# Performance work log

Hardware: AMD Instinct MI355X
Metric: run time of the kernel (lower is better)

## Reference

```python
import jax, jax.numpy as jnp
from jax import lax
import numpy as np

B = 16; C1 = 96; H4 = 28; W4 = 64
FULL_H = 448; FULL_W = 1024
BACKWARP = 1.25   # fltBackwarp for intLevel=4
SCALE = 16.0      # 2**intLevel
MD = 4            # correlation max displacement -> (2*MD+1)**2 = 81 channels


def _lrelu(x):
    return jnp.where(x >= 0, x, 0.1 * x)


def _conv3(x, w, b):
    y = lax.conv_general_dilated(x, w, (1, 1), [(1, 1), (1, 1)],
                                 dimension_numbers=('NCHW', 'OIHW', 'NCHW'))
    return y + b[None, :, None, None]


def _deconv4s2(x, w, b):
    # PyTorch ConvTranspose2d(k=4, s=2, p=1); w has PyTorch layout (in, out, kH, kW)
    wt = jnp.transpose(w[:, :, ::-1, ::-1], (1, 0, 2, 3))  # flipped, (out, in, kH, kW)
    y = lax.conv_general_dilated(x, wt, (1, 1), [(2, 2), (2, 2)],
                                 lhs_dilation=(2, 2),
                                 dimension_numbers=('NCHW', 'OIHW', 'NCHW'))
    return y + b[None, :, None, None]


def _correlation(f1, f2):
    # Channel-mean cost volume over a (2*MD+1)^2 displacement window.
    b, c, h, w = f1.shape
    f2p = jnp.pad(f2, ((0, 0), (0, 0), (MD, MD), (MD, MD)))
    vols = [jnp.mean(f1 * f2p[:, :, dy:dy + h, dx:dx + w], axis=1)
            for dy in range(2 * MD + 1) for dx in range(2 * MD + 1)]
    return jnp.stack(vols, axis=1)  # [B, 81, H, W]


def _warp(feat, flow):
    # Bilinear backward warp with zero padding outside the image.
    b, c, h, w = feat.shape
    gy, gx = jnp.meshgrid(jnp.arange(h, dtype=feat.dtype),
                          jnp.arange(w, dtype=feat.dtype), indexing='ij')
    x = gx[None] + flow[:, 0]
    y = gy[None] + flow[:, 1]
    x0 = jnp.floor(x); y0 = jnp.floor(y)
    wx = x - x0; wy = y - y0
    feat_flat = feat.reshape(b, c, h * w)

    def gather(yi, xi):
        valid = ((yi >= 0) & (yi <= h - 1) & (xi >= 0) & (xi <= w - 1)).astype(feat.dtype)
        yc = jnp.clip(yi, 0, h - 1).astype(jnp.int32)
        xc = jnp.clip(xi, 0, w - 1).astype(jnp.int32)
        idx = (yc * w + xc).reshape(b, 1, h * w)
        g = jnp.take_along_axis(feat_flat, jnp.broadcast_to(idx, (b, c, h * w)), axis=2)
        return g.reshape(b, c, h, w) * valid[:, None]

    return (gather(y0, x0) * ((1 - wy) * (1 - wx))[:, None]
            + gather(y0, x0 + 1) * ((1 - wy) * wx)[:, None]
            + gather(y0 + 1, x0) * (wy * (1 - wx))[:, None]
            + gather(y0 + 1, x0 + 1) * (wy * wx)[:, None])


def _quat_to_mat(q):
    # (w, x, y, z) quaternion -> rotation matrix, pytorch3d convention.
    q = q / jnp.linalg.norm(q, axis=-1, keepdims=True)
    w, x, y, z = q[:, 0], q[:, 1], q[:, 2], q[:, 3]
    R = jnp.stack([
        1 - 2 * (y * y + z * z), 2 * (x * y - w * z),     2 * (x * z + w * y),
        2 * (x * y + w * z),     1 - 2 * (x * x + z * z), 2 * (y * z - w * x),
        2 * (x * z - w * y),     2 * (y * z + w * x),     1 - 2 * (x * x + y * y)
    ], axis=-1).reshape(-1, 3, 3)
    return R


def _rot_flow(R, K, Kinv, h, w):
    # Rotational flow: p' = K R K^{-1} p (homogeneous), flow = p'/z - p.
    gy, gx = jnp.meshgrid(jnp.arange(h, dtype=R.dtype),
                          jnp.arange(w, dtype=R.dtype), indexing='ij')
    p = jnp.stack([gx.ravel(), gy.ravel(), jnp.ones(h * w, dtype=R.dtype)], axis=0)  # [3, HW]
    M = jnp.einsum('ij,bjk,kl->bil', K, R, Kinv)  # [B,3,3]
    pp = jnp.einsum('bij,jn->bin', M, p)
    pp2 = pp[:, :2] / pp[:, 2:3]
    return (pp2 - p[None, :2]).reshape(-1, 2, h, w)


def setup_inputs():
    key = jax.random.key(0)
    ks = jax.random.split(key, 24)

    def rnd(i, shape, scale=1.0):
        return scale * jax.random.normal(ks[i], shape, dtype=jnp.float32)

    def wconv(i, cout, cin, k=3):
        return rnd(i, (cout, cin, k, k), (2.0 / (cin * k * k)) ** 0.5)

    K = np.array([[500.0, 0.0, FULL_W / 2.0],
                  [0.0, 500.0, FULL_H / 2.0],
                  [0.0, 0.0, 1.0]], dtype=np.float32)
    quat = jnp.concatenate([jnp.ones((B, 1), jnp.float32), 0.01 * rnd(0, (B, 3))], axis=1)
    return {
        'tenOne': rnd(1, (B, C1, H4, W4)),
        'tenTwo': rnd(2, (B, C1, H4, W4)),
        'prev_flow': rnd(3, (B, 2, H4 // 2, W4 // 2)),
        'prev_feat': rnd(4, (B, 663, H4 // 2, W4 // 2)),
        'rotation_quat': quat,
        'cam_intri': jnp.asarray(K),
        'cam_intri_inv': jnp.asarray(np.linalg.inv(K)),
        'upflow_w': rnd(5, (2, 2, 4, 4), 0.1),
        'upflow_b': jnp.zeros((2,), jnp.float32),
        'upfeat_w': rnd(6, (663, 2, 4, 4), 0.02),
        'upfeat_b': jnp.zeros((2,), jnp.float32),
        'w1': wconv(7, 128, 183), 'b1': jnp.zeros((128,), jnp.float32),
        'w2': wconv(8, 128, 311), 'b2': jnp.zeros((128,), jnp.float32),
        'w3': wconv(9, 96, 439),  'b3': jnp.zeros((96,), jnp.float32),
        'w4': wconv(10, 64, 535), 'b4': jnp.zeros((64,), jnp.float32),
        'w5': wconv(11, 32, 599), 'b5': jnp.zeros((32,), jnp.float32),
        'w6': wconv(12, 2, 631),  'b6': jnp.zeros((2,), jnp.float32),
        'height': FULL_H,
        'width': FULL_W,
    }


def reference(tenOne, tenTwo, prev_flow, prev_feat, rotation_quat, cam_intri, cam_intri_inv,
              upflow_w, upflow_b, upfeat_w, upfeat_b,
              w1, b1, w2, b2, w3, b3, w4, b4, w5, b5, w6, b6, height, width):
    rh, rw = height // 16, width // 16  # 2**intLevel = 16
    delt_R = _quat_to_mat(rotation_quat)
    R_flow = _rot_flow(delt_R, cam_intri, cam_intri_inv, height, width)
    R_flow_r = jax.image.resize(R_flow, (R_flow.shape[0], 2, rh, rw), method='bilinear') / SCALE
    tenTwo_w = _warp(tenTwo, R_flow_r)
    tenFlow = _deconv4s2(prev_flow, upflow_w, upflow_b)
    tenFeatUp = _deconv4s2(prev_feat, upfeat_w, upfeat_b)
    tenVolume = _lrelu(_correlation(tenOne, _warp(tenTwo_w, tenFlow * BACKWARP)))
    feat = jnp.concatenate([tenVolume, R_flow_r, tenOne, tenFlow, tenFeatUp], axis=1)  # 183 ch
    for wc, bc in ((w1, b1), (w2, b2), (w3, b3), (w4, b4), (w5, b5)):
        feat = jnp.concatenate([_lrelu(_conv3(feat, wc, bc)), feat], axis=1)
    tenFlow_out = _lrelu(_conv3(feat, w6, b6))
    return tenFlow_out, feat
```

## Files before the change

kernel.cpp:

```cpp
#include <hip/hip_runtime.h>
#include <cstdint>
#include <cstddef>

typedef unsigned short u16;
typedef __attribute__((ext_vector_type(8))) short  short8;
typedef __attribute__((ext_vector_type(4))) float  f32x4;

#define HW4   1792
#define FCH   631
#define OUTOFF ((size_t)57344)

__device__ __forceinline__ float b2f(u16 u){
  union { unsigned int i; float f; } v; v.i = ((unsigned int)u) << 16; return v.f;
}
__device__ __forceinline__ u16 f2b(float f){
  unsigned int x = __float_as_uint(f);
  return (u16)((x + 0x7fffu + ((x >> 16) & 1u)) >> 16);
}
__device__ __forceinline__ float lrelu(float v){ return v >= 0.f ? v : 0.1f * v; }
__device__ __forceinline__ bool is_f32(const void* probe){ return ((const float*)probe)[0] > 1.0f; }
__device__ __forceinline__ float ldg_(const void* p, size_t i, bool f){
  return f ? ((const float*)p)[i] : b2f(((const u16*)p)[i]);
}
__device__ __forceinline__ void stg_(void* p, size_t i, float v, bool f){
  if (f) ((float*)p)[i] = v; else ((u16*)p)[i] = f2b(v);
}
__device__ __forceinline__ short8 zero8(){
  union { long long l[2]; short8 s; } z; z.l[0] = 0; z.l[1] = 0; return z.s;
}
__device__ __forceinline__ f32x4 zero4(){
  union { long long l[2]; f32x4 s; } z; z.l[0] = 0; z.l[1] = 0; return z.s;
}
__device__ __forceinline__ short8 swap16(short8 v){
  union { short8 s; unsigned int u[4]; } a, r;
  a.s = v;
  #pragma unroll
  for (int i = 0; i < 4; i++) r.u[i] = (a.u[i] >> 16) | (a.u[i] << 16);
  return r.s;
}

__global__ void k_M(const void* __restrict__ quat, const void* __restrict__ K,
                    const void* __restrict__ Kinv, float* __restrict__ Mout){
  bool f = is_f32(K);
  int b = threadIdx.x;
  if (b >= 16) return;
  float q0 = ldg_(quat,b*4+0,f), q1 = ldg_(quat,b*4+1,f);
  float q2 = ldg_(quat,b*4+2,f), q3 = ldg_(quat,b*4+3,f);
  float n = sqrtf(q0*q0 + q1*q1 + q2*q2 + q3*q3);
  float w = q0/n, x = q1/n, y = q2/n, z = q3/n;
  float R[9];
  R[0] = 1.f - 2.f*(y*y + z*z); R[1] = 2.f*(x*y - w*z); R[2] = 2.f*(x*z + w*y);
  R[3] = 2.f*(x*y + w*z); R[4] = 1.f - 2.f*(x*x + z*z); R[5] = 2.f*(y*z - w*x);
  R[6] = 2.f*(x*z - w*y); R[7] = 2.f*(y*z + w*x); R[8] = 1.f - 2.f*(x*x + y*y);
  float Kf[9], Ki[9];
  for (int i = 0; i < 9; i++){ Kf[i] = ldg_(K,i,f); Ki[i] = ldg_(Kinv,i,f); }
  float T[9];
  for (int r = 0; r < 3; r++)
    for (int c = 0; c < 3; c++)
      T[r*3+c] = R[r*3+0]*Ki[0*3+c] + R[r*3+1]*Ki[1*3+c] + R[r*3+2]*Ki[2*3+c];
  for (int r = 0; r < 3; r++)
    for (int c = 0; c < 3; c++)
      Mout[b*9 + r*3 + c] = Kf[r*3+0]*T[0*3+c] + Kf[r*3+1]*T[1*3+c] + Kf[r*3+2]*T[2*3+c];
}

__global__ void k_rflow_col(const float* __restrict__ Mws, float* __restrict__ tmpA){
  int t = blockIdx.x * 256 + threadIdx.x;
  int xo = t & 63;
  int yf = (t >> 6) % 448;
  int b  = t / (448*64);
  const float* M = Mws + b*9;
  float m0=M[0],m1=M[1],m2=M[2],m3=M[3],m4=M[4],m5=M[5],m6=M[6],m7=M[7],m8=M[8];
  float cx = 16.f*xo + 7.5f;
  float yff = (float)yf;
  float su = 0.f, sv = 0.f, wsum = 0.f;
  for (int i = 0; i < 32; i++){
    int xi = 16*xo - 8 + i;
    if (xi < 0 || xi > 1023) continue;
    float xf = (float)xi;
    float wgt = 1.f - fabsf(xf - cx) * (1.f/16.f);
    float den = m6*xf + m7*yff + m8;
    float inv = 1.f / den;
    float u = (m0*xf + m1*yff + m2)*inv - xf;
    float v = (m3*xf + m4*yff + m5)*inv - yff;
    su += wgt*u; sv += wgt*v; wsum += wgt;
  }
  float rn = 1.f / wsum;
  tmpA[((size_t)(b*2+0)*64 + xo)*448 + yf] = su*rn;
  tmpA[((size_t)(b*2+1)*64 + xo)*448 + yf] = sv*rn;
}

__global__ void k_rflow_row(const float* __restrict__ tmpA, float* __restrict__ rfr,
                            void* __restrict__ outb, const void* probe){
  bool f = is_f32(probe);
  int t = blockIdx.x * 256 + threadIdx.x;
  int xo = t & 63;
  int yo = (t >> 6) % 28;
  int b  = t / HW4;
  float cy = 16.f*yo + 7.5f;
  for (int c = 0; c < 2; c++){
    const float* col = tmpA + ((size_t)(b*2+c)*64 + xo)*448;
    float s = 0.f, wsum = 0.f;
    for (int i = 0; i < 32; i++){
      int yi = 16*yo - 8 + i;
      if (yi < 0 || yi > 447) continue;
      float wgt = 1.f - fabsf((float)yi - cy) * (1.f/16.f);
      s += wgt * col[yi]; wsum += wgt;
    }
    float val = s / (wsum * 16.0f);
    rfr[(size_t)(b*2+c)*HW4 + yo*64 + xo] = val;
    stg_(outb, OUTOFF + ((size_t)b*FCH + 529 + c)*HW4 + yo*64 + xo, val, f);
  }
}

__global__ void k_dflow(const void* __restrict__ pf, const void* __restrict__ w,
                        const void* __restrict__ bias, float* __restrict__ tflow,
                        void* __restrict__ outb, const void* probe){
  bool f = is_f32(probe);
  int t = blockIdx.x * 256 + threadIdx.x;
  int x = t & 63;
  int y = (t >> 6) % 28;
  int co = (t / HW4) & 1;
  int b  = t / (2*HW4);
  float acc = ldg_(bias, co, f);
  for (int ky = 0; ky < 4; ky++){
    int dy = y + ky - 2;
    if (dy < 0 || dy > 26 || (dy & 1)) continue;
    int iy = dy >> 1;
    for (int kx = 0; kx < 4; kx++){
      int dx = x + kx - 2;
      if (dx < 0 || dx > 62 || (dx & 1)) continue;
      int ix = dx >> 1;
      for (int ci = 0; ci < 2; ci++){
        acc += ldg_(pf, ((size_t)(b*2+ci)*14 + iy)*32 + ix, f) *
               ldg_(w,  (size_t)ci*32 + co*16 + (3-ky)*4 + (3-kx), f);
      }
    }
  }
  tflow[(size_t)(b*2+co)*HW4 + y*64 + x] = acc;
  stg_(outb, OUTOFF + ((size_t)b*FCH + 627 + co)*HW4 + y*64 + x, acc, f);
}

#define DF_NCH 42
__global__ __launch_bounds__(256) void k_dfeat_s1(
    const void* __restrict__ pfeat, const void* __restrict__ w,
    float* __restrict__ part, const void* probe){
  bool f = is_f32(probe);
  __shared__ float s_in[16*448];
  __shared__ float s_w[16*32];
  const int tid = threadIdx.x;
  const int ch = blockIdx.x;
  const int b  = blockIdx.y;
  if (f){
    const float* src = (const float*)pfeat + ((size_t)b*663 + (size_t)ch*16)*448;
    #pragma unroll
    for (int i = 0; i < 7; i++){
      int e = tid + 256*i;
      int ci = ch*16 + e/112;
      float4 v = {0.f,0.f,0.f,0.f};
      if (ci < 663) v = *(const float4*)(src + e*4);
      *(float4*)&s_in[e*4] = v;
    }
  } else {
    const u16* src = (const u16*)pfeat + ((size_t)b*663 + (size_t)ch*16)*448;
    #pragma unroll
    for (int i = 0; i < 7; i++){
      int e = tid + 256*i;
      int ci = ch*16 + e/112;
      float4 v = {0.f,0.f,0.f,0.f};
      if (ci < 663){
        ushort4 u = *(const ushort4*)(src + e*4);
        v.x = b2f(u.x); v.y = b2f(u.y); v.z = b2f(u.z); v.w = b2f(u.w);
      }
      *(float4*)&s_in[e*4] = v;
    }
  }
  #pragma unroll
  for (int i = 0; i < 2; i++){
    int e = tid + 256*i;
    int ci = ch*16 + (e >> 5);
    s_w[e] = (ci < 663) ? ldg_(w, (size_t)ci*32 + (e & 31), f) : 0.f;
  }
  __syncthreads();
  const int x = tid & 63;
  int ix0=-1, ix1=-1, wx0=0, wx1=0;
  { int n = 0;
    for (int kx = (x & 1); kx < 4; kx += 2){
      int dx = x + kx - 2;
      if (dx >= 0 && dx <= 62){
        if (n == 0){ ix0 = dx >> 1; wx0 = 3-kx; } else { ix1 = dx >> 1; wx1 = 3-kx; }
        n++;
      }
    } }
  float* pout = part + (size_t)(b*DF_NCH + ch)*2*1792;
  #pragma unroll
  for (int i = 0; i < 7; i++){
    int p = tid + 256*i;
    int y = p >> 6;
    int iy0=-1, iy1=-1, wy0=0, wy1=0;
    { int n = 0;
      for (int ky = (y & 1); ky < 4; ky += 2){
        int dy = y + ky - 2;
        if (dy >= 0 && dy <= 26){
          if (n == 0){ iy0 = dy >> 1; wy0 = (3-ky)*4; } else { iy1 = dy >> 1; wy1 = (3-ky)*4; }
          n++;
        }
      } }
    const bool v00 = (iy0 >= 0) && (ix0 >= 0);
    const bool v01 = (iy0 >= 0) && (ix1 >= 0);
    const bool v10 = (iy1 >= 0) && (ix0 >= 0);
    const bool v11 = (iy1 >= 0) && (ix1 >= 0);
    const int o00 = iy0*32+ix0, o01 = iy0*32+ix1, o10 = iy1*32+ix0, o11 = iy1*32+ix1;
    const int w00 = wy0+wx0, w01 = wy0+wx1, w10 = wy1+wx0, w11 = wy1+wx1;
    float a0 = 0.f, a1 = 0.f;
    #pragma unroll 4
    for (int ci = 0; ci < 16; ci++){
      const float* si = s_in + ci*448;
      const float* sw = s_w + ci*32;
      if (v00){ float iv = si[o00]; a0 += iv*sw[w00]; a1 += iv*sw[16+w00]; }
      if (v01){ float iv = si[o01]; a0 += iv*sw[w01]; a1 += iv*sw[16+w01]; }
      if (v10){ float iv = si[o10]; a0 += iv*sw[w10]; a1 += iv*sw[16+w10]; }
      if (v11){ float iv = si[o11]; a0 += iv*sw[w11]; a1 += iv*sw[16+w11]; }
    }
    pout[p]        = a0;
    pout[1792 + p] = a1;
  }
}

__global__ void k_dfeat_s2(const float* __restrict__ part, const void* __restrict__ bias,
                           void* __restrict__ outb, const void* probe){
  bool f = is_f32(probe);
  int t = blockIdx.x * 256 + threadIdx.x;
  int x = t & 63;
  int y = (t >> 6) % 28;
  int co = (t / HW4) & 1;
  int b  = t / (2*HW4);
  float s = ldg_(bias, co, f);
  const float* pp = part + ((size_t)b*(2*DF_NCH) + co)*1792 + (size_t)(y*64 + x);
  #pragma unroll
  for (int ch = 0; ch < DF_NCH; ch++) s += pp[(size_t)ch*3584];
  stg_(outb, OUTOFF + ((size_t)b*FCH + 629 + co)*HW4 + y*64 + x, s, f);
}

__global__ void k_copy_one(const void* __restrict__ one, void* __restrict__ outb,
                           const void* probe){
  bool f = is_f32(probe);
  int t = blockIdx.x * 256 + threadIdx.x;
  int p = t % HW4;
  int c = (t / HW4) % 96;
  int b = t / (96*HW4);
  stg_(outb, OUTOFF + ((size_t)b*FCH + 531 + c)*HW4 + p,
       ldg_(one, (size_t)(b*96+c)*HW4 + p, f), f);
}

__global__ void k_warp2(const void* __restrict__ two, const float* __restrict__ rfr,
                        const float* __restrict__ tflow, float* __restrict__ wrp2,
                        const void* probe){
  bool f = is_f32(probe);
  int t = blockIdx.x * 256 + threadIdx.x;
  int x = t & 63;
  int y = (t >> 6) % 28;
  int c = (t / HW4) % 96;
  int b = t / (96*HW4);
  float qu = tflow[(size_t)(b*2+0)*HW4 + y*64 + x] * 1.25f;
  float qv = tflow[(size_t)(b*2+1)*HW4 + y*64 + x] * 1.25f;
  float qx = (float)x + qu, qy = (float)y + qv;
  float qx0 = floorf(qx), qy0 = floorf(qy);
  float wx = qx - qx0, wy = qy - qy0;
  const size_t cb = (size_t)(b*96+c)*HW4;
  float acc = 0.f;
  #pragma unroll
  for (int a = 0; a < 2; a++){
    #pragma unroll
    for (int bb = 0; bb < 2; bb++){
      float ry = qy0 + (float)a, rx = qx0 + (float)bb;
      if (ry < 0.f || ry > 27.f || rx < 0.f || rx > 63.f) continue;
      float W = (a ? wy : 1.f-wy) * (bb ? wx : 1.f-wx);
      int iry = (int)ry, irx = (int)rx;
      float su = rfr[(size_t)(b*2+0)*HW4 + iry*64 + irx];
      float sv = rfr[(size_t)(b*2+1)*HW4 + iry*64 + irx];
      float sx = rx + su, sy = ry + sv;
      float sx0 = floorf(sx), sy0 = floorf(sy);
      float swx = sx - sx0, swy = sy - sy0;
      float inner = 0.f;
      #pragma unroll
      for (int aa = 0; aa < 2; aa++){
        #pragma unroll
        for (int cc2 = 0; cc2 < 2; cc2++){
          float gy2 = sy0 + (float)aa, gx2 = sx0 + (float)cc2;
          if (gy2 < 0.f || gy2 > 27.f || gx2 < 0.f || gx2 > 63.f) continue;
          float wv = (aa ? swy : 1.f-swy) * (cc2 ? swx : 1.f-swx);
          inner += wv * ldg_(two, cb + (size_t)((int)gy2*64 + (int)gx2), f);
        }
      }
      acc += W * inner;
    }
  }
  wrp2[t] = acc;
}

__global__ void k_corr(const void* __restrict__ one, const float* __restrict__ two,
                       void* __restrict__ outb, const void* probe){
  bool f = is_f32(probe);
  int t = blockIdx.x * 256 + threadIdx.x;
  int x  = t & 63;
  int y  = (t >> 6) % 28;
  int dy = (t / HW4) % 9;
  int b  = t / (9*HW4);
  float acc[9];
  #pragma unroll
  for (int i = 0; i < 9; i++) acc[i] = 0.f;
  int row = y + dy - 4;
  if (row >= 0 && row < 28){
    for (int c = 0; c < 96; c++){
      float f1 = ldg_(one, (size_t)(b*96+c)*HW4 + y*64 + x, f);
      const float* rp = two + (size_t)(b*96+c)*HW4 + row*64;
      #pragma unroll
      for (int dx = 0; dx < 9; dx++){
        int xx = x + dx - 4;
        if (xx >= 0 && xx < 64) acc[dx] += f1 * rp[xx];
      }
    }
  }
  #pragma unroll
  for (int dx = 0; dx < 9; dx++){
    float v = lrelu(acc[dx] * (1.f/96.f));
    stg_(outb, OUTOFF + ((size_t)b*FCH + 448 + dy*9 + dx)*HW4 + y*64 + x, v, f);
  }
}

__global__ __launch_bounds__(256) void k_conv(
    void* __restrict__ base, size_t in_off,
    const void* __restrict__ w, const void* __restrict__ bias,
    int Cin, int Cout, size_t out_off, size_t out_bstr, const void* probe,
    int bf16_only){
  bool f = is_f32(probe);
  if (bf16_only && f) return;
  __shared__ float s_in[32*3*66];
  __shared__ float s_w[32*9*32];
  int tid = threadIdx.x;
  int x = tid & 63;
  int g = tid >> 6;
  int by = blockIdx.x;
  int b = by / 28, y = by % 28;
  int co_base = blockIdx.y * 32;
  const size_t FB = (size_t)FCH * HW4;
  float acc[8];
  #pragma unroll
  for (int j = 0; j < 8; j++) acc[j] = 0.f;

  for (int ci0 = 0; ci0 < Cin; ci0 += 32){
    int cc = min(32, Cin - ci0);
    if (f){
      const float* inb = (const float*)base + in_off + (size_t)b*FB;
      for (int e = tid; e < cc*198; e += 256){
        int ci = e / 198; int rem = e - ci*198;
        int r = rem / 66; int xx = rem - r*66;
        int iy = y + r - 1; int ix = xx - 1;
        float v = 0.f;
        if (iy >= 0 && iy < 28 && ix >= 0 && ix < 64)
          v = inb[(size_t)(ci0+ci)*HW4 + iy*64 + ix];
        s_in[(ci*3 + r)*66 + xx] = v;
      }
      const float* wf = (const float*)w;
      for (int e = tid; e < cc*288; e += 256){
        int co_i = e & 31; int k = (e >> 5) % 9; int ci = e / 288;
        int co = co_base + co_i;
        float v = 0.f;
        if (co < Cout) v = wf[((size_t)co*Cin + ci0 + ci)*9 + k];
        s_w[(ci*9 + k)*32 + co_i] = v;
      }
    } else {
      const u16* inb = (const u16*)base + in_off + (size_t)b*FB;
      for (int e = tid; e < cc*198; e += 256){
        int ci = e / 198; int rem = e - ci*198;
        int r = rem / 66; int xx = rem - r*66;
        int iy = y + r - 1; int ix = xx - 1;
        float v = 0.f;
        if (iy >= 0 && iy < 28 && ix >= 0 && ix < 64)
          v = b2f(inb[(size_t)(ci0+ci)*HW4 + iy*64 + ix]);
        s_in[(ci*3 + r)*66 + xx] = v;
      }
      const u16* wf = (const u16*)w;
      for (int e = tid; e < cc*288; e += 256){
        int co_i = e & 31; int k = (e >> 5) % 9; int ci = e / 288;
        int co = co_base + co_i;
        float v = 0.f;
        if (co < Cout) v = b2f(wf[((size_t)co*Cin + ci0 + ci)*9 + k]);
        s_w[(ci*9 + k)*32 + co_i] = v;
      }
    }
    __syncthreads();
    for (int ci = 0; ci < cc; ci++){
      const float* si = &s_in[ci*198 + x];
      const float* sw = &s_w[ci*288 + 8*g];
      #pragma unroll
      for (int ky = 0; ky < 3; ky++){
        #pragma unroll
        for (int kx = 0; kx < 3; kx++){
          float v = si[ky*66 + kx];
          const float* wp = sw + (ky*3 + kx)*32;
          float4 wa = *(const float4*)(wp);
          float4 wb = *(const float4*)(wp + 4);
          acc[0] += wa.x*v; acc[1] += wa.y*v; acc[2] += wa.z*v; acc[3] += wa.w*v;
          acc[4] += wb.x*v; acc[5] += wb.y*v; acc[6] += wb.z*v; acc[7] += wb.w*v;
        }
      }
    }
    __syncthreads();
  }
  #pragma unroll
  for (int j = 0; j < 8; j++){
    int co = co_base + 8*g + j;
    if (co < Cout){
      float v = lrelu(acc[j] + ldg_(bias, co, f));
      stg_(base, out_off + (size_t)b*out_bstr + (size_t)co*HW4 + y*64 + x, v, f);
    }
  }
}

__global__ void k_wprep(const void* __restrict__ w, u16* __restrict__ wT,
                        int Cin, int Cout, int nCB, int total, const void* probe){
  if (!is_f32(probe)) return;
  int t = blockIdx.x * 256 + threadIdx.x;
  if (t >= total) return;
  int j     = t & 7;
  int lane  = (t >> 3) & 63;
  int rest  = t >> 9;
  int tI    = rest & 3;
  int rest2 = rest >> 2;
  int tap   = rest2 % 9;
  int gc    = rest2 / 9;
  int cb    = gc % nCB;
  int gyb   = gc / nCB;
  int kk = ((lane >> 4) << 3) + j;
  int ci = cb*16 + (kk >> 1);
  int co = gyb*64 + tI*16 + (lane & 15);
  float x = 0.f;
  if (co < Cout && ci < Cin) x = ((const float*)w)[((size_t)co*Cin + ci)*9 + tap];
  u16 hi = f2b(x);
  wT[t] = (kk & 1) ? f2b(x - b2f(hi)) : hi;
}

__global__ __launch_bounds__(256, 2) void k_conv_ms(
    void* __restrict__ base, size_t in_off, const u16* __restrict__ wT,
    const void* __restrict__ bias, int Cin, int nCB, int Cout,
    size_t out_off, size_t out_bstr, const void* __restrict__ probe){
  if (!is_f32(probe)) return;
  __shared__ __align__(16) u16 lds[26624];
  const int tid  = threadIdx.x;
  const int lane = tid & 63, wv = tid >> 6;
  const int lx = lane & 15, lg = lane >> 4;
  const int wr  = wv & 1;
  const int wxh = wv >> 1;
  const int b  = blockIdx.x & 15;
  const int y0 = (blockIdx.x >> 4) * 2;
  const int coB = (int)blockIdx.y * 64;
  const float* inb = (const float*)base + in_off + (size_t)b * ((size_t)FCH * HW4);
  const u16* wTg = wT + (size_t)blockIdx.y * (size_t)nCB * 18432;

  f32x4 acc[4][2];
  #pragma unroll
  for (int tI = 0; tI < 4; tI++){ acc[tI][0] = zero4(); acc[tI][1] = zero4(); }

  int offb[3];
  #pragma unroll
  for (int kx = 0; kx < 3; kx++){
    int xo = lx + kx - 1;
    offb[kx] = (xo >> 4)*512 + (xo & 15)*32 + ((lg ^ ((xo >> 2) & 3)) << 3);
  }
  const bool maskB0 = (lx == 0  && wxh == 0);
  const bool maskB1 = (lx == 15 && wxh == 1);

  const int sx4 = tid & 15;
  const int sr  = (tid >> 4) & 3;
  const int srow = y0 - 1 + sr;
  const bool rok = (srow >= 0 && srow < 28);
  const int swz = sx4 & 3;
  const int nb0 = sr*64 + sx4*4;

  float4 paA[4], paB[4];
  short8 pwA[9], pwB[9];

  auto LOADA = [&](int cb){
    const u16* wsrc = wTg + (size_t)cb * 18432;
    #pragma unroll
    for (int i = 0; i < 9; i++)
      pwA[i] = *(const short8*)(wsrc + (size_t)(wv*9 + i)*512 + lane*8);
    #pragma unroll
    for (int i = 0; i < 4; i++){
      int ci = cb*16 + wv + 4*i;
      float4 v = {0.f, 0.f, 0.f, 0.f};
      if (rok && ci < Cin) v = *(const float4*)(inb + (size_t)ci*HW4 + srow*64 + sx4*4);
      paA[i] = v;
    }
  };
  auto LOADB = [&](int cb){
    const u16* wsrc = wTg + (size_t)cb * 18432;
    #pragma unroll
    for (int i = 0; i < 9; i++)
      pwB[i] = *(const short8*)(wsrc + (size_t)(wv*9 + i)*512 + lane*8);
    #pragma unroll
    for (int i = 0; i < 4; i++){
      int ci = cb*16 + wv + 4*i;
      float4 v = {0.f, 0.f, 0.f, 0.f};
      if (rok && ci < Cin) v = *(const float4*)(inb + (size_t)ci*HW4 + srow*64 + sx4*4);
      paB[i] = v;
    }
  };
  auto WRITEA = [&](){
    #pragma unroll
    for (int i = 0; i < 9; i++)
      *(short8*)&lds[8192 + (wv*9 + i)*512 + lane*8] = pwA[i];
    #pragma unroll
    for (int i = 0; i < 4; i++){
      int cil = wv + 4*i;
      int jo = (((cil >> 2) ^ swz) << 3) + 2*(cil & 3);
      #pragma unroll
      for (int u = 0; u < 4; u++){
        float xv = (&paA[i].x)[u];
        u16 hi = f2b(xv);
        u16 lo = f2b(xv - b2f(hi));
        *(unsigned int*)&lds[(nb0 + u)*32 + jo] = (unsigned int)hi | ((unsigned int)lo << 16);
      }
    }
  };
  auto WRITEB = [&](){
    #pragma unroll
    for (int i = 0; i < 9; i++)
      *(short8*)&lds[8192 + (wv*9 + i)*512 + lane*8] = pwB[i];
    #pragma unroll
    for (int i = 0; i < 4; i++){
      int cil = wv + 4*i;
      int jo = (((cil >> 2) ^ swz) << 3) + 2*(cil & 3);
      #pragma unroll
      for (int u = 0; u < 4; u++){
        float xv = (&paB[i].x)[u];
        u16 hi = f2b(xv);
        u16 lo = f2b(xv - b2f(hi));
        *(unsigned int*)&lds[(nb0 + u)*32 + jo] = (unsigned int)hi | ((unsigned int)lo << 16);
      }
    }
  };
  auto COMPUTE = [&](){
    #pragma unroll
    for (int ky = 0; ky < 3; ky++){
      const int rb = (wr + ky)*2048 + wxh*1024;
      #pragma unroll
      for (int kx = 0; kx < 3; kx++){
        const int k = ky*3 + kx;
        const int bA = rb + offb[kx];
        short8 B0 = *(const short8*)&lds[bA];
        short8 B1 = *(const short8*)&lds[bA + 512];
        if (kx == 0 && maskB0) B0 = zero8();
        if (kx == 2 && maskB1) B1 = zero8();
        short8 S0 = swap16(B0), S1 = swap16(B1);
        #pragma unroll
        for (int tI = 0; tI < 4; tI++){
          short8 Af = *(const short8*)&lds[8192 + ((k*4 + tI)*64 + lane)*8];
          acc[tI][0] = __builtin_amdgcn_mfma_f32_16x16x32_bf16(Af, B0, acc[tI][0], 0,0,0);
          acc[tI][0] = __builtin_amdgcn_mfma_f32_16x16x32_bf16(Af, S0, acc[tI][0], 0,0,0);
          acc[tI][1] = __builtin_amdgcn_mfma_f32_16x16x32_bf16(Af, B1, acc[tI][1], 0,0,0);
          acc[tI][1] = __builtin_amdgcn_mfma_f32_16x16x32_bf16(Af, S1, acc[tI][1], 0,0,0);
        }
      }
    }
  };

  LOADA(0);
  for (int cb = 0; cb < nCB; cb += 2){
    WRITEA();
    LOADB(cb + 1);
    __syncthreads();
    COMPUTE();
    __syncthreads();
    WRITEB();
    if (cb + 2 < nCB) LOADA(cb + 2);
    __syncthreads();
    COMPUTE();
    __syncthreads();
  }
  float* ob = (float*)base;
  const float* bf = (const float*)bias;
  const int y = y0 + wr;
  #pragma unroll
  for (int tI = 0; tI < 4; tI++){
    #pragma unroll
    for (int xg = 0; xg < 2; xg++){
      const int x = wxh*32 + xg*16 + lx;
      #pragma unroll
      for (int r4 = 0; r4 < 4; r4++){
        int co = coB + tI*16 + lg*4 + r4;
        if (co < Cout){
          float v = lrelu(acc[tI][xg][r4] + bf[co]);
          ob[out_off + (size_t)b*out_bstr + (size_t)co*HW4 + (size_t)(y*64 + x)] = v;
        }
      }
    }
  }
}

extern "C" void kernel_launch(void* const* d_in, const int* in_sizes, int n_in,
                              void* d_out, int out_size, void* d_ws, size_t ws_size,
                              hipStream_t stream){
  const void* tenOne    = d_in[0];
  const void* tenTwo    = d_in[1];
  const void* prev_flow = d_in[2];
  const void* prev_feat = d_in[3];
  const void* quat      = d_in[4];
  const void* K         = d_in[5];
  const void* Kinv      = d_in[6];
  const void* upflow_w  = d_in[7];
  const void* upflow_b  = d_in[8];
  const void* upfeat_w  = d_in[9];
  const void* upfeat_b  = d_in[10];
  const void* w1 = d_in[11];  const void* b1 = d_in[12];
  const void* w2 = d_in[13];  const void* b2 = d_in[14];
  const void* w3 = d_in[15];  const void* b3 = d_in[16];
  const void* w4 = d_in[17];  const void* b4 = d_in[18];
  const void* w5 = d_in[19];  const void* b5 = d_in[20];
  const void* w6 = d_in[21];  const void* b6 = d_in[22];
  const void* probe = K;

  float* ws    = (float*)d_ws;
  float* Mws   = ws;
  float* tmpA  = ws + 160;
  float* rfr   = ws + 917664;
  float* tflow = ws + 975008;
  float* wrp2  = ws + 1032352;
  u16*   wTb   = (u16*)(ws + 3784864);
  float* dpart = wrp2;

  const bool ws_ok = ws_size >= (size_t)23691904;

  k_M<<<1, 64, 0, stream>>>(quat, K, Kinv, Mws);
  k_rflow_col<<<1792, 256, 0, stream>>>(Mws, tmpA);
  k_rflow_row<<<112, 256, 0, stream>>>(tmpA, rfr, d_out, probe);
  k_dflow<<<224, 256, 0, stream>>>(prev_flow, upflow_w, upflow_b, tflow, d_out, probe);
  k_dfeat_s1<<<dim3(DF_NCH, 16), 256, 0, stream>>>(prev_feat, upfeat_w, dpart, probe);
  k_dfeat_s2<<<224, 256, 0, stream>>>(dpart, upfeat_b, d_out, probe);
  k_copy_one<<<10752, 256, 0, stream>>>(tenOne, d_out, probe);
  k_warp2<<<10752, 256, 0, stream>>>(tenTwo, rfr, tflow, wrp2, probe);
  k_corr<<<1008, 256, 0, stream>>>(tenOne, wrp2, d_out, probe);

  const size_t FB = (size_t)FCH * HW4;
  const size_t f0 = OUTOFF;

  struct LD { const void *w, *bi; int Cin, Cout, nCB, gy; size_t wOff, in_off, out_off, out_bstr; };
  const LD L[6] = {
    { w1, b1, 183, 128, 12, 2, 0,       f0+(size_t)448*HW4, f0+(size_t)320*HW4, FB },
    { w2, b2, 311, 128, 20, 2, 442368,  f0+(size_t)320*HW4, f0+(size_t)192*HW4, FB },
    { w3, b3, 439,  96, 28, 2, 1179648, f0+(size_t)192*HW4, f0+(size_t) 96*HW4, FB },
    { w4, b4, 535,  64, 34, 1, 2211840, f0+(size_t) 96*HW4, f0+(size_t) 32*HW4, FB },
    { w5, b5, 599,  32, 38, 1, 2838528, f0+(size_t) 32*HW4, f0,                 FB },
    { w6, b6, 631,   2, 40, 1, 3538944, f0,                 0,        (size_t)2*HW4 },
  };

  if (ws_ok){
    for (int i = 0; i < 6; i++){
      int total = L[i].gy * L[i].nCB * 18432;
      k_wprep<<<(total + 255)/256, 256, 0, stream>>>(
          L[i].w, wTb + L[i].wOff, L[i].Cin, L[i].Cout, L[i].nCB, total, probe);
    }
    for (int i = 0; i < 6; i++){
      k_conv_ms<<<dim3(224, L[i].gy), 256, 0, stream>>>(
          d_out, L[i].in_off, wTb + L[i].wOff, L[i].bi,
          L[i].Cin, L[i].nCB, L[i].Cout,
          L[i].out_off, L[i].out_bstr, probe);
    }
  }
  const int bf16_only = ws_ok ? 1 : 0;
  k_conv<<<dim3(448,4), 256, 0, stream>>>(d_out, f0 + (size_t)448*HW4, w1, b1, 183, 128,
                                          f0 + (size_t)320*HW4, FB, probe, bf16_only);
  k_conv<<<dim3(448,4), 256, 0, stream>>>(d_out, f0 + (size_t)320*HW4, w2, b2, 311, 128,
                                          f0 + (size_t)192*HW4, FB, probe, bf16_only);
  k_conv<<<dim3(448,3), 256, 0, stream>>>(d_out, f0 + (size_t)192*HW4, w3, b3, 439, 96,
                                          f0 + (size_t)96*HW4, FB, probe, bf16_only);
  k_conv<<<dim3(448,2), 256, 0, stream>>>(d_out, f0 + (size_t)96*HW4, w4, b4, 535, 64,
                                          f0 + (size_t)32*HW4, FB, probe, bf16_only);
  k_conv<<<dim3(448,1), 256, 0, stream>>>(d_out, f0 + (size_t)32*HW4, w5, b5, 599, 32,
                                          f0, FB, probe, bf16_only);
  k_conv<<<dim3(448,1), 256, 0, stream>>>(d_out, f0, w6, b6, 631, 2,
                                          0, (size_t)2*HW4, probe, bf16_only);
}
```

Baseline: 927.1 us.

## Template conv on output-tile count and split Cout across more blocks

The MFMA conv kernel is templated on the number of 16-wide output-channel tiles per block (2 or 1 instead of 4), so each layer launches more blocks along the output-channel axis and uses smaller LDS and register footprints. Launch bounds rise to allow 3 blocks per SM. The input staging is rewritten so each thread loads one pixel across 16 channels and writes a single swizzled 16-byte LDS vector. The aim is more parallelism and occupancy for the narrow late layers. The cost is more blocks re-reading the same input tile and less weight reuse per input load.

Measured after the change: 857.3 us. 1.08x faster.

```diff
diff --git a/kernel.cpp b/kernel.cpp
--- a/kernel.cpp
+++ b/kernel.cpp
@@ -37,6 +37,10 @@
   #pragma unroll
   for (int i = 0; i < 4; i++) r.u[i] = (a.u[i] >> 16) | (a.u[i] << 16);
   return r.s;
+}
+__device__ __forceinline__ void split2(float x, u16& h, u16& l){
+  h = f2b(x);
+  l = f2b(x - b2f(h));
 }
 
 __global__ void k_M(const void* __restrict__ quat, const void* __restrict__ K,
@@ -419,34 +423,38 @@
 }
 
 __global__ void k_wprep(const void* __restrict__ w, u16* __restrict__ wT,
-                        int Cin, int Cout, int nCB, int total, const void* probe){
+                        int Cin, int Cout, int nCB, int nTI, int total, const void* probe){
   if (!is_f32(probe)) return;
   int t = blockIdx.x * 256 + threadIdx.x;
   if (t >= total) return;
   int j     = t & 7;
   int lane  = (t >> 3) & 63;
   int rest  = t >> 9;
-  int tI    = rest & 3;
-  int rest2 = rest >> 2;
-  int tap   = rest2 % 9;
-  int gc    = rest2 / 9;
+  int tI    = rest % nTI;
+  int r2    = rest / nTI;
+  int tap   = r2 % 9;
+  int gc    = r2 / 9;
   int cb    = gc % nCB;
   int gyb   = gc / nCB;
   int kk = ((lane >> 4) << 3) + j;
   int ci = cb*16 + (kk >> 1);
-  int co = gyb*64 + tI*16 + (lane & 15);
+  int co = gyb*nTI*16 + tI*16 + (lane & 15);
   float x = 0.f;
   if (co < Cout && ci < Cin) x = ((const float*)w)[((size_t)co*Cin + ci)*9 + tap];
   u16 hi = f2b(x);
   wT[t] = (kk & 1) ? f2b(x - b2f(hi)) : hi;
 }
 
-__global__ __launch_bounds__(256, 2) void k_conv_ms(
+template<int NTI>
+__global__ __launch_bounds__(256, 3) void k_conv_ms(
     void* __restrict__ base, size_t in_off, const u16* __restrict__ wT,
     const void* __restrict__ bias, int Cin, int nCB, int Cout,
     size_t out_off, size_t out_bstr, const void* __restrict__ probe){
   if (!is_f32(probe)) return;
-  __shared__ __align__(16) u16 lds[26624];
+  constexpr int WU16 = 9*NTI*512;
+  constexpr int WCH  = WU16/8;
+  constexpr int NW   = (WCH + 255)/256;
+  __shared__ __align__(16) u16 lds[8192 + WU16];
   const int tid  = threadIdx.x;
   const int lane = tid & 63, wv = tid >> 6;
   const int lx = lane & 15, lg = lane >> 4;
@@ -454,13 +462,13 @@
   const int wxh = wv >> 1;
   const int b  = blockIdx.x & 15;
   const int y0 = (blockIdx.x >> 4) * 2;
-  const int coB = (int)blockIdx.y * 64;
+  const int coB = (int)blockIdx.y * (NTI*16);
   const float* inb = (const float*)base + in_off + (size_t)b * ((size_t)FCH * HW4);
-  const u16* wTg = wT + (size_t)blockIdx.y * (size_t)nCB * 18432;
-
-  f32x4 acc[4][2];
-  #pragma unroll
-  for (int tI = 0; tI < 4; tI++){ acc[tI][0] = zero4(); acc[tI][1] = zero4(); }
+  const u16* wTg = wT + (size_t)blockIdx.y * (size_t)nCB * WU16;
+
+  f32x4 acc[NTI][2];
+  #pragma unroll
+  for (int tI = 0; tI < NTI; tI++){ acc[tI][0] = zero4(); acc[tI][1] = zero4(); }
 
   int offb[3];
   #pragma unroll
@@ -471,74 +479,80 @@
   const bool maskB0 = (lx == 0  && wxh == 0);
   const bool maskB1 = (lx == 15 && wxh == 1);
 
-  const int sx4 = tid & 15;
-  const int sr  = (tid >> 4) & 3;
-  const int srow = y0 - 1 + sr;
+  const int sx   = tid & 63;
+  const int srow = y0 - 1 + (tid >> 6);
   const bool rok = (srow >= 0 && srow < 28);
-  const int swz = sx4 & 3;
-  const int nb0 = sr*64 + sx4*4;
-
-  float4 paA[4], paB[4];
-  short8 pwA[9], pwB[9];
+  const int sw4  = (tid >> 2) & 3;
+
+  float paA[16], paB[16];
+  short8 pwA[NW], pwB[NW];
 
   auto LOADA = [&](int cb){
-    const u16* wsrc = wTg + (size_t)cb * 18432;
-    #pragma unroll
-    for (int i = 0; i < 9; i++)
-      pwA[i] = *(const short8*)(wsrc + (size_t)(wv*9 + i)*512 + lane*8);
-    #pragma unroll
-    for (int i = 0; i < 4; i++){
-      int ci = cb*16 + wv + 4*i;
-      float4 v = {0.f, 0.f, 0.f, 0.f};
-      if (rok && ci < Cin) v = *(const float4*)(inb + (size_t)ci*HW4 + srow*64 + sx4*4);
-      paA[i] = v;
-    }
+    const u16* wsrc = wTg + (size_t)cb * WU16;
+    #pragma unroll
+    for (int i = 0; i < NW; i++){
+      int e = tid + 256*i;
+      if (e < WCH) pwA[i] = *(const short8*)(wsrc + (size_t)e*8);
+    }
+    #pragma unroll
+    for (int i = 0; i < 4; i++)
+      #pragma unroll
+      for (int c = 0; c < 4; c++){
+        int ci = cb*16 + i*4 + c;
+        float v = 0.f;
+        if (rok && ci < Cin) v = inb[(size_t)ci*HW4 + srow*64 + sx];
+        paA[i*4+c] = v;
+      }
   };
   auto LOADB = [&](int cb){
-    const u16* wsrc = wTg + (size_t)cb * 18432;
-    #pragma unroll
-    for (int i = 0; i < 9; i++)
-      pwB[i] = *(const short8*)(wsrc + (size_t)(wv*9 + i)*512 + lane*8);
-    #pragma unroll
-    for (int i = 0; i < 4; i++){
-      int ci = cb*16 + wv + 4*i;
-      float4 v = {0.f, 0.f, 0.f, 0.f};
-      if (rok && ci < Cin) v = *(const float4*)(inb + (size_t)ci*HW4 + srow*64 + sx4*4);
-      paB[i] = v;
-    }
+    const u16* wsrc = wTg + (size_t)cb * WU16;
+    #pragma unroll
+    for (int i = 0; i < NW; i++){
+      int e = tid + 256*i;
+      if (e < WCH) pwB[i] = *(const short8*)(wsrc + (size_t)e*8);
+    }
+    #pragma unroll
+    for (int i = 0; i < 4; i++)
+      #pragma unroll
+      for (int c = 0; c < 4; c++){
+        int ci = cb*16 + i*4 + c;
+        float v = 0.f;
+        if (rok && ci < Cin) v = inb[(size_t)ci*HW4 + srow*64 + sx];
+        paB[i*4+c] = v;
+      }
   };
   auto WRITEA = [&](){
     #pragma unroll
-    for (int i = 0; i < 9; i++)
-      *(short8*)&lds[8192 + (wv*9 + i)*512 + lane*8] = pwA[i];
+    for (int i = 0; i < NW; i++){
+      int e = tid + 256*i;
+      if (e < WCH) *(short8*)&lds[8192 + e*8] = pwA[i];
+    }
     #pragma unroll
     for (int i = 0; i < 4; i++){
-      int cil = wv + 4*i;
-      int jo = (((cil >> 2) ^ swz) << 3) + 2*(cil & 3);
-      #pragma unroll
-      for (int u = 0; u < 4; u++){
-        float xv = (&paA[i].x)[u];
-        u16 hi = f2b(xv);
-        u16 lo = f2b(xv - b2f(hi));
-        *(unsigned int*)&lds[(nb0 + u)*32 + jo] = (unsigned int)hi | ((unsigned int)lo << 16);
-      }
+      short8 s;
+      #pragma unroll
+      for (int c = 0; c < 4; c++){
+        u16 h, l; split2(paA[i*4+c], h, l);
+        s[2*c] = (short)h; s[2*c+1] = (short)l;
+      }
+      *(short8*)&lds[tid*32 + ((i ^ sw4) << 3)] = s;
     }
   };
   auto WRITEB = [&](){
     #pragma unroll
-    for (int i = 0; i < 9; i++)
-      *(short8*)&lds[8192 + (wv*9 + i)*512 + lane*8] = pwB[i];
+    for (int i = 0; i < NW; i++){
+      int e = tid + 256*i;
+      if (e < WCH) *(short8*)&lds[8192 + e*8] = pwB[i];
+    }
     #pragma unroll
     for (int i = 0; i < 4; i++){
-      int cil = wv + 4*i;
-      int jo = (((cil >> 2) ^ swz) << 3) + 2*(cil & 3);
-      #pragma unroll
-      for (int u = 0; u < 4; u++){
-        float xv = (&paB[i].x)[u];
-        u16 hi = f2b(xv);
-        u16 lo = f2b(xv - b2f(hi));
-        *(unsigned int*)&lds[(nb0 + u)*32 + jo] = (unsigned int)hi | ((unsigned int)lo << 16);
-      }
+      short8 s;
+      #pragma unroll
+      for (int c = 0; c < 4; c++){
+        u16 h, l; split2(paB[i*4+c], h, l);
+        s[2*c] = (short)h; s[2*c+1] = (short)l;
+      }
+      *(short8*)&lds[tid*32 + ((i ^ sw4) << 3)] = s;
     }
   };
   auto COMPUTE = [&](){
@@ -555,8 +569,8 @@
         if (kx == 2 && maskB1) B1 = zero8();
         short8 S0 = swap16(B0), S1 = swap16(B1);
         #pragma unroll
-        for (int tI = 0; tI < 4; tI++){
-          short8 Af = *(const short8*)&lds[8192 + ((k*4 + tI)*64 + lane)*8];
+        for (int tI = 0; tI < NTI; tI++){
+          short8 Af = *(const short8*)&lds[8192 + ((k*NTI + tI)*64 + lane)*8];
           acc[tI][0] = __builtin_amdgcn_mfma_f32_16x16x32_bf16(Af, B0, acc[tI][0], 0,0,0);
           acc[tI][0] = __builtin_amdgcn_mfma_f32_16x16x32_bf16(Af, S0, acc[tI][0], 0,0,0);
           acc[tI][1] = __builtin_amdgcn_mfma_f32_16x16x32_bf16(Af, B1, acc[tI][1], 0,0,0);
@@ -583,7 +597,7 @@
   const float* bf = (const float*)bias;
   const int y = y0 + wr;
   #pragma unroll
-  for (int tI = 0; tI < 4; tI++){
+  for (int tI = 0; tI < NTI; tI++){
     #pragma unroll
     for (int xg = 0; xg < 2; xg++){
       const int x = wxh*32 + xg*16 + lx;
@@ -630,7 +644,7 @@
   u16*   wTb   = (u16*)(ws + 3784864);
   float* dpart = wrp2;
 
-  const bool ws_ok = ws_size >= (size_t)23691904;
+  const bool ws_ok = ws_size >= (size_t)21369472;
 
   k_M<<<1, 64, 0, stream>>>(quat, K, Kinv, Mws);
   k_rflow_col<<<1792, 256, 0, stream>>>(Mws, tmpA);
@@ -645,27 +659,32 @@
   const size_t FB = (size_t)FCH * HW4;
   const size_t f0 = OUTOFF;
 
-  struct LD { const void *w, *bi; int Cin, Cout, nCB, gy; size_t wOff, in_off, out_off, out_bstr; };
+  struct LD { const void *w, *bi; int Cin, Cout, nCB, gy, nTI;
+              size_t wOff, in_off, out_off, out_bstr; };
   const LD L[6] = {
-    { w1, b1, 183, 128, 12, 2, 0,       f0+(size_t)448*HW4, f0+(size_t)320*HW4, FB },
-    { w2, b2, 311, 128, 20, 2, 442368,  f0+(size_t)320*HW4, f0+(size_t)192*HW4, FB },
-    { w3, b3, 439,  96, 28, 2, 1179648, f0+(size_t)192*HW4, f0+(size_t) 96*HW4, FB },
-    { w4, b4, 535,  64, 34, 1, 2211840, f0+(size_t) 96*HW4, f0+(size_t) 32*HW4, FB },
-    { w5, b5, 599,  32, 38, 1, 2838528, f0+(size_t) 32*HW4, f0,                 FB },
-    { w6, b6, 631,   2, 40, 1, 3538944, f0,                 0,        (size_t)2*HW4 },
+    { w1, b1, 183, 128, 12, 4, 2, 0,       f0+(size_t)448*HW4, f0+(size_t)320*HW4, FB },
+    { w2, b2, 311, 128, 20, 4, 2, 442368,  f0+(size_t)320*HW4, f0+(size_t)192*HW4, FB },
+    { w3, b3, 439,  96, 28, 3, 2, 1179648, f0+(size_t)192*HW4, f0+(size_t) 96*HW4, FB },
+    { w4, b4, 535,  64, 34, 2, 2, 1953792, f0+(size_t) 96*HW4, f0+(size_t) 32*HW4, FB },
+    { w5, b5, 599,  32, 38, 2, 1, 2580480, f0+(size_t) 32*HW4, f0,                 FB },
+    { w6, b6, 631,   2, 40, 1, 1, 2930688, f0,                 0,        (size_t)2*HW4 },
   };
 
   if (ws_ok){
     for (int i = 0; i < 6; i++){
-      int total = L[i].gy * L[i].nCB * 18432;
+      int total = L[i].gy * L[i].nCB * 9 * L[i].nTI * 512;
       k_wprep<<<(total + 255)/256, 256, 0, stream>>>(
-          L[i].w, wTb + L[i].wOff, L[i].Cin, L[i].Cout, L[i].nCB, total, probe);
+          L[i].w, wTb + L[i].wOff, L[i].Cin, L[i].Cout, L[i].nCB, L[i].nTI, total, probe);
     }
     for (int i = 0; i < 6; i++){
-      k_conv_ms<<<dim3(224, L[i].gy), 256, 0, stream>>>(
-          d_out, L[i].in_off, wTb + L[i].wOff, L[i].bi,
-          L[i].Cin, L[i].nCB, L[i].Cout,
-          L[i].out_off, L[i].out_bstr, probe);
+      if (L[i].nTI == 2)
+        k_conv_ms<2><<<dim3(224, L[i].gy), 256, 0, stream>>>(
+            d_out, L[i].in_off, wTb + L[i].wOff, L[i].bi,
+            L[i].Cin, L[i].nCB, L[i].Cout, L[i].out_off, L[i].out_bstr, probe);
+      else
+        k_conv_ms<1><<<dim3(224, L[i].gy), 256, 0, stream>>>(
+            d_out, L[i].in_off, wTb + L[i].wOff, L[i].bi,
+            L[i].Cin, L[i].nCB, L[i].Cout, L[i].out_off, L[i].out_bstr, probe);
     }
   }
   const int bf16_only = ws_ok ? 1 : 0;
```
